# Kernel optimization log

Measured on AMD Instinct MI355X. Metric: run time of the kernel, lower is better.

Reference implementation:

```python
import jax, jax.numpy as jnp
import numpy as np

B, S, D, G, N_ORIG = 4, 4096, 512, 64, 4096
EPS_NORM = 1e-12   # F.normalize eps
EPS_MERGE = 1e-8   # merge-weight eps


def setup_inputs() -> dict:
    key = jax.random.key(0)
    k1, k2, k3 = jax.random.split(key, 3)
    x = jax.random.normal(k1, (B, S, D), dtype=jnp.float32)
    source = jax.random.uniform(k2, (B, S, N_ORIG), dtype=jnp.float32)
    position_ids = jnp.arange(B * S, dtype=jnp.int64).reshape(B, S)
    W = jax.random.normal(k3, (D, G), dtype=jnp.float32) * 0.05  # group_proj weight (no bias)
    return {"x": x, "source": source, "position_ids": position_ids,
            "r": 1024, "window_size": 16, "W": W}


def _token_merge(x, source, position_ids, r, window_size, W):
    Bb, Ss, Dd = x.shape
    r = min(r, Ss // 2)
    idx = jnp.arange(Ss, dtype=jnp.int32)
    # local candidate pairs: |i-j| = d for d in 1..window_size-1
    pi = jnp.concatenate([idx[:Ss - d] for d in range(1, min(window_size, Ss))])
    pj = jnp.concatenate([idx[d:] for d in range(1, min(window_size, Ss))])

    g = x @ W                                   # (B,S,G)
    norms = jnp.linalg.norm(g, axis=-1)         # (B,S)
    gn = g / jnp.maximum(norms, EPS_NORM)[..., None]
    sim = jnp.einsum('bpg,bpg->bp', gn[:, pi], gn[:, pj])  # (B,P)

    def greedy(sim_b):
        # deterministic order: score DESC, i ASC, j ASC
        order = jnp.lexsort((pj, pi, -sim_b))
        oi, oj = pi[order], pj[order]

        def step(carry, ij):
            used, partner, cnt = carry
            i, j = ij
            take = (cnt < r) & (~used[i]) & (~used[j])
            used = used.at[i].set(used[i] | take).at[j].set(used[j] | take)
            partner = partner.at[i].set(jnp.where(take, j, partner[i]))
            cnt = cnt + take.astype(jnp.int32)
            return (used, partner, cnt), None

        init = (jnp.zeros(Ss, bool), jnp.full(Ss, -1, jnp.int32), jnp.int32(0))
        (used, partner, cnt), _ = jax.lax.scan(step, init, (oi, oj))
        return partner  # partner[i] = j if pair (i,j) selected, else -1

    partner = jax.vmap(greedy)(sim)  # (B,S)

    def merge(xb, sb, pb, partner_b, norms_b):
        sel = partner_b >= 0
        pj_safe = jnp.where(sel, partner_b, idx)
        wi = norms_b
        wj = jnp.where(sel, norms_b[pj_safe], 0.0)
        merged = (wi[:, None] * xb + wj[:, None] * xb[pj_safe]) / (wi + wj + EPS_MERGE)[:, None]
        x_m = jnp.where(sel[:, None], merged, xb)
        s_m = sb + jnp.where(sel, 1.0, 0.0)[:, None] * sb[pj_safe]
        # drop the second token of each merged pair, preserving order
        skip_idx = jnp.where(sel, partner_b, Ss)
        skip = jnp.zeros(Ss, bool).at[skip_idx].set(True, mode='drop')
        keep = jnp.argsort(skip.astype(jnp.int8), stable=True)[: Ss - r]
        return x_m[keep], s_m[keep], pb[keep]

    return jax.vmap(merge)(x, source, position_ids, partner, norms)


def reference(x, source, position_ids, r, window_size, W):
    return _token_merge(x, source, position_ids, r, window_size, W)
```

## Files before the change

### kernel.cpp

```cpp
#include <hip/hip_runtime.h>

#define BATCH 4
#define SLEN 4096
#define DDIM 512
#define GDIM 64
#define NORIG 4096
#define WMAX 15
#define RSEL 1024
#define KEEP (SLEN - RSEL)
#define NTOK (BATCH * SLEN)
#define PEEL_ROUNDS 256
#define LDSL 16

typedef float __attribute__((ext_vector_type(4))) f32x4;

#define OFF_LISTS ((size_t)0)
#define OFF_GN    ((size_t)0)
#define OFF_SIMST ((size_t)8388608)
#define OFF_NORMS ((size_t)10485760)
#define OFF_KT    ((size_t)10584064)
#define OFF_PJR   ((size_t)10633216)
#define OFF_WIR   ((size_t)10682368)
#define OFF_WJR   ((size_t)10731520)
#define WS_NEEDED ((size_t)10780672)

#define OUTX_OFF 0
#define OUTS_OFF 6291456
#define OUTP_OFF 56623104

__global__ __launch_bounds__(256) void k_proj(const float* __restrict__ x,
                                              const float* __restrict__ Wm,
                                              double* __restrict__ gn,
                                              float* __restrict__ norms) {
  __shared__ float xs[16 * DDIM];
  int base = blockIdx.x * 16;
  const float4* src = (const float4*)(x + (size_t)base * DDIM);
  float4* dstv = (float4*)xs;
  for (int idx = threadIdx.x; idx < 16 * DDIM / 4; idx += 256) dstv[idx] = src[idx];
  __syncthreads();
  int lane = threadIdx.x & 63;
  int wv = threadIdx.x >> 6;
  double acc0 = 0, acc1 = 0, acc2 = 0, acc3 = 0;
  const float* xw = xs + wv * 4 * DDIM;
  for (int d = 0; d < DDIM; ++d) {
    double wval = (double)Wm[d * GDIM + lane];
    acc0 += (double)xw[d] * wval;
    acc1 += (double)xw[DDIM + d] * wval;
    acc2 += (double)xw[2 * DDIM + d] * wval;
    acc3 += (double)xw[3 * DDIM + d] * wval;
  }
  double accs[4] = {acc0, acc1, acc2, acc3};
  for (int k = 0; k < 4; ++k) {
    double a = accs[k];
    double ss = a * a;
    for (int o = 32; o >= 1; o >>= 1) ss += __shfl_xor(ss, o, 64);
    double nrm = sqrt(ss);
    int tok = base + wv * 4 + k;
    if (lane == 0) norms[tok] = (float)nrm;
    double denom = nrm > 1e-12 ? nrm : 1e-12;
    gn[(size_t)tok * GDIM + lane] = a / denom;
  }
}

__global__ __launch_bounds__(256) void k_sims(const double* __restrict__ gn,
                                              double* __restrict__ simsT) {
  int blk = blockIdx.x;
  int b = blk >> 6;
  int t0 = (blk & 63) * 64;
  int nrows = min(64 + WMAX, SLEN - t0);
  __shared__ double gs[(64 + WMAX) * GDIM];
  const double* src = gn + ((size_t)b * SLEN + t0) * GDIM;
  for (int idx = threadIdx.x; idx < nrows * GDIM; idx += 256) gs[idx] = src[idx];
  __syncthreads();
  int lane = threadIdx.x & 63, wv = threadIdx.x >> 6;
  for (int s = wv; s < 64 * WMAX; s += 4) {
    int il = s & 63, d = (s >> 6) + 1;
    int i = t0 + il;
    if (i + d < SLEN) {
      double p = gs[il * GDIM + lane] * gs[(il + d) * GDIM + lane];
      for (int o = 32; o >= 1; o >>= 1) p += __shfl_xor(p, o, 64);
      if (lane == 0) simsT[((size_t)(b * SLEN + i)) * 16 + d] = p;
    }
  }
}

__global__ __launch_bounds__(256) void k_lists(const double* __restrict__ simsT,
                                               signed char* __restrict__ lists8) {
  __shared__ signed char stage[4][32];
  int wave = threadIdx.x >> 6, lane = threadIdx.x & 63;
  int t = blockIdx.x * 4 + wave;
  int b = t >> 12, tt = t & (SLEN - 1);
  const double* sb = simsT + (size_t)b * SLEN * 16;
  int d = (lane >> 1) + 1;
  int side = lane & 1;
  bool valid = (lane < 30) && (side == 0 ? (tt + d < SLEN) : (tt - d >= 0));
  unsigned long long key = 0ULL;
  unsigned int code = 0xFFFFu;
  signed char delta = 0;
  if (valid) {
    int i = (side == 0) ? tt : (tt - d);
    double s = sb[(size_t)i * 16 + d];
    unsigned long long bits = (unsigned long long)__double_as_longlong(s);
    key = (bits & 0x8000000000000000ULL) ? ~bits : (bits | 0x8000000000000000ULL);
    code = (unsigned int)((i << 4) | d);
    delta = (side == 0) ? (signed char)d : (signed char)(-d);
  }
  int rank = 0;
#pragma clang loop unroll(disable)
  for (int q = 0; q < 30; ++q) {
    unsigned long long kq = __shfl(key, q, 64);
    unsigned int cq = __shfl(code, q, 64);
    if (kq != 0ULL && (kq > key || (kq == key && cq < code))) rank++;
  }
  if (lane < 32) stage[wave][lane] = 0;
  if (valid) stage[wave][rank] = delta;
  if (lane < 32) lists8[(size_t)t * 32 + lane] = stage[wave][lane];
}

__global__ __launch_bounds__(1024) void k_match(const signed char* __restrict__ lists8,
                                                const double* __restrict__ simsT_all,
                                                const float* __restrict__ norms,
                                                int* __restrict__ kt, int* __restrict__ pjr,
                                                float* __restrict__ wir, float* __restrict__ wjr,
                                                float* __restrict__ out_pos) {
  int b = blockIdx.x;
  const signed char* lb = lists8 + (size_t)b * SLEN * 32;
  const double* simsT = simsT_all + (size_t)b * SLEN * 16;
  __shared__ __align__(16) unsigned char big[65536];
  __shared__ signed char bp[SLEN];
  __shared__ unsigned char used[SLEN];
  __shared__ unsigned char cur[SLEN];
  __shared__ unsigned short takenCode[2048];
  __shared__ unsigned char meta[SLEN];
  __shared__ int takenCnt, baseCnt;
  __shared__ int sharedB, sharedNeed, sdone, allAccept, smallStraddle;
  __shared__ int memberCnt;
  __shared__ int wTot[16], wOff[16];
  signed char* l8 = (signed char*)big;
  int tid = threadIdx.x;

#pragma clang loop unroll(disable)
  for (int t = tid; t < SLEN; t += 1024) {
    const unsigned long long* lp = (const unsigned long long*)(lb + (size_t)t * 32);
    unsigned long long v0 = lp[0], v1 = lp[1];
    unsigned long long* dp = (unsigned long long*)(l8 + t * LDSL);
    dp[0] = v0; dp[1] = v1;
    bp[t] = (signed char)(v0 & 0xFF);
    used[t] = 0; cur[t] = 0; meta[t] = 0;
  }
  if (tid == 0) takenCnt = 0;
  __syncthreads();

#pragma clang loop unroll(disable)
  for (int round = 0; round < PEEL_ROUNDS; ++round) {
    if (tid == 0) baseCnt = takenCnt;
    __syncthreads();
#pragma clang loop unroll(disable)
    for (int t = tid; t < SLEN; t += 1024) {
      int dlt = bp[t];
      if (dlt > 0 && !used[t]) {
        int j = t + dlt;
        if (!used[j] && bp[j] == (signed char)(-dlt)) {
          int idx = atomicAdd(&takenCnt, 1);
          if (idx < 2048) takenCode[idx] = (unsigned short)((t << 4) | dlt);
          used[t] = 1; used[j] = 1;
        }
      }
    }
    __syncthreads();
    int newCnt = takenCnt;
    if (newCnt == baseCnt) break;
#pragma clang loop unroll(disable)
    for (int t = tid; t < SLEN; t += 1024) {
      if (used[t]) { bp[t] = 0; continue; }
      int dlt = bp[t];
      if (dlt == 0) continue;
      int p = t + dlt;
      int cc = cur[t];
#pragma clang loop unroll(disable)
      while (dlt != 0 && used[p]) {
        ++cc;
        dlt = (cc < LDSL) ? l8[t * LDSL + cc]
            : ((cc < 32) ? lb[(size_t)t * 32 + cc] : (signed char)0);
        p = t + dlt;
      }
      cur[t] = (unsigned char)cc;
      bp[t] = (signed char)dlt;
    }
    __syncthreads();
  }

  unsigned long long* key = (unsigned long long*)big;
  unsigned short* codeA = (unsigned short*)(big + 16384);
  unsigned char* state = (unsigned char*)(big + 20480);
  unsigned int* hist = (unsigned int*)(big + 22528);
  unsigned int* bcum = (unsigned int*)(big + 23552);
  unsigned int* wsum = (unsigned int*)(big + 24576);
  unsigned short* memberIdx = (unsigned short*)(big + 24704);
  int m = min(takenCnt, 2048);
  __syncthreads();
#pragma clang loop unroll(disable)
  for (int k = tid; k < m; k += 1024) {
    unsigned short c = takenCode[k];
    codeA[k] = c;
    state[k] = 0;
    double s = simsT[(size_t)(c >> 4) * 16 + (c & 15)];
    unsigned long long bits = (unsigned long long)__double_as_longlong(s);
    key[k] = (bits & 0x8000000000000000ULL) ? ~bits : (bits | 0x8000000000000000ULL);
  }
  if (tid == 0) { sharedNeed = RSEL; sdone = 0; allAccept = (m <= RSEL); smallStraddle = 0; memberCnt = 0; }
  __syncthreads();

  if (!allAccept) {
#pragma clang loop unroll(disable)
    for (int pass = 0; pass < 8; ++pass) {
      if (tid < 256) hist[tid] = 0;
      __syncthreads();
      int sh = 56 - 8 * pass;
#pragma clang loop unroll(disable)
      for (int k = tid; k < m; k += 1024)
        if (!state[k]) atomicAdd(&hist[(unsigned int)(key[k] >> sh) & 0xFFu], 1u);
      __syncthreads();
      unsigned int v = 0, inc = 0;
      int lane = tid & 63, w = tid >> 6;
      if (tid < 256) {
        v = hist[255 - tid];
        inc = v;
        for (int o = 1; o < 64; o <<= 1) { unsigned int n = __shfl_up(inc, o, 64); if (lane >= o) inc += n; }
        if (lane == 63) wsum[w] = inc;
      }
      __syncthreads();
      if (tid < 256) {
        unsigned int off = 0;
        for (int ww = 0; ww < w; ++ww) off += wsum[ww];
        unsigned int incl = inc + off;
        bcum[255 - tid] = incl - v;
      }
      __syncthreads();
      if (tid < 256) {
        int bkt = 255 - tid;
        unsigned int ag = bcum[bkt];
        unsigned int need = (unsigned int)sharedNeed;
        if (ag < need && ag + hist[bkt] >= need) sharedB = bkt;
      }
      __syncthreads();
      int B = sharedB;
      unsigned int needInB = (unsigned int)sharedNeed - bcum[B];
#pragma clang loop unroll(disable)
      for (int k = tid; k < m; k += 1024) {
        if (!state[k]) {
          unsigned int bv = (unsigned int)(key[k] >> sh) & 0xFFu;
          if ((int)bv > B) state[k] = 1;
          else if ((int)bv < B) state[k] = 2;
        }
      }
      __syncthreads();
      if (tid == 0) {
        sharedNeed = (int)needInB;
        if (hist[B] == needInB) sdone = 1;
        else if (hist[B] <= 128) smallStraddle = 1;
      }
      __syncthreads();
      if (sdone || smallStraddle) break;
    }
  }
  __syncthreads();

  if (allAccept || sdone) {
#pragma clang loop unroll(disable)
    for (int k = tid; k < m; k += 1024) if (!state[k]) state[k] = 1;
  } else {
#pragma clang loop unroll(disable)
    for (int k = tid; k < m; k += 1024)
      if (!state[k]) { int idx = atomicAdd(&memberCnt, 1); memberIdx[idx] = (unsigned short)k; }
    __syncthreads();
    int mc = memberCnt;
    unsigned int need = (unsigned int)sharedNeed;
#pragma clang loop unroll(disable)
    for (int z = tid; z < mc; z += 1024) {
      int k = memberIdx[z];
      unsigned long long kk = key[k];
      unsigned short ck = codeA[k];
      unsigned int wr = 0;
#pragma clang loop unroll(disable)
      for (int q2 = 0; q2 < mc; ++q2) {
        int q = memberIdx[q2];
        unsigned long long kq = key[q];
        if (kq > kk || (kq == kk && codeA[q] < ck)) wr++;
      }
      if (wr < need) state[k] = 1;
    }
  }
  __syncthreads();
#pragma clang loop unroll(disable)
  for (int k = tid; k < m; k += 1024) {
    if (state[k] == 1) {
      unsigned short ck = codeA[k];
      int i = ck >> 4, d = ck & 15;
      meta[i] = (unsigned char)d;
      meta[i + d] = 0x80;
    }
  }
  __syncthreads();
  int cnt = 0; unsigned char kf[4];
  int tbase = tid * 4;
  for (int u = 0; u < 4; ++u) { kf[u] = (meta[tbase + u] & 0x80) ? 0 : 1; cnt += kf[u]; }
  int lane = tid & 63, wv = tid >> 6;
  int incl = cnt;
  for (int o = 1; o < 64; o <<= 1) { int n = __shfl_up(incl, o, 64); if (lane >= o) incl += n; }
  if (lane == 63) wTot[wv] = incl;
  __syncthreads();
  if (tid < 16) {
    int v2 = wTot[tid];
    for (int o = 1; o < 16; o <<= 1) { int n = __shfl_up(v2, o, 64); if (lane >= o) v2 += n; }
    wOff[tid] = v2 - wTot[tid];
  }
  __syncthreads();
  int pos = wOff[wv] + (incl - cnt);
  for (int u = 0; u < 4; ++u) {
    int t = tbase + u;
    if (kf[u]) {
      if (pos < KEEP) {
        int orow = b * KEEP + pos;
        kt[orow] = t;
        int d = meta[t] & 15;
        pjr[orow] = d ? (t + d) : -1;
        wir[orow] = norms[b * SLEN + t];
        wjr[orow] = d ? norms[b * SLEN + t + d] : 0.0f;
        out_pos[orow] = (float)(b * SLEN + t);
      }
      pos++;
    }
  }
}

__global__ __launch_bounds__(256) void k_gather(const float* __restrict__ x,
                                                const float* __restrict__ src,
                                                const int* __restrict__ kt, const int* __restrict__ pjr,
                                                const float* __restrict__ wir, const float* __restrict__ wjr,
                                                float* __restrict__ outx, float* __restrict__ outs) {
  int orow = blockIdx.x;
  int b = orow / KEEP;
  int t = kt[orow], pj = pjr[orow];
  int gi = min(max(b * SLEN + t, 0), NTOK - 1);
  int gj = min(b * SLEN + min(max(pj, 0), SLEN - 1), NTOK - 1);
  int c = threadIdx.x;
  if (c < 128) {
    const f32x4* xi = (const f32x4*)(x + (size_t)gi * DDIM);
    f32x4 v = __builtin_nontemporal_load(&xi[c]);
    if (pj >= 0) {
      const f32x4* xj = (const f32x4*)(x + (size_t)gj * DDIM);
      f32x4 u = __builtin_nontemporal_load(&xj[c]);
      float wi = wir[orow], wj = wjr[orow];
      float inv = 1.0f / (wi + wj + 1e-8f);
      v = (v * wi + u * wj) * inv;
    }
    __builtin_nontemporal_store(v, (f32x4*)(outx + (size_t)orow * DDIM) + c);
  }
  const f32x4* si = (const f32x4*)(src + (size_t)gi * NORIG);
  f32x4* o = (f32x4*)(outs + (size_t)orow * NORIG);
  if (pj >= 0) {
    const f32x4* sj = (const f32x4*)(src + (size_t)gj * NORIG);
    for (int u = 0; u < 4; ++u) {
      int c2 = c + u * 256;
      f32x4 a = __builtin_nontemporal_load(&si[c2]);
      f32x4 bb = __builtin_nontemporal_load(&sj[c2]);
      __builtin_nontemporal_store(a + bb, &o[c2]);
    }
  } else {
    for (int u = 0; u < 4; ++u) {
      int c2 = c + u * 256;
      f32x4 a = __builtin_nontemporal_load(&si[c2]);
      __builtin_nontemporal_store(a, &o[c2]);
    }
  }
}

extern "C" void kernel_launch(void* const* d_in, const int* in_sizes, int n_in,
                              void* d_out, int out_size, void* d_ws, size_t ws_size,
                              hipStream_t stream) {
  if (ws_size < WS_NEEDED) return;

  const float* x = (const float*)d_in[0];
  const float* source = (const float*)d_in[1];
  const float* Wm = (const float*)d_in[5];

  char* ws = (char*)d_ws;
  double* gn = (double*)(ws + OFF_GN);
  double* simsT = (double*)(ws + OFF_SIMST);
  float* norms = (float*)(ws + OFF_NORMS);
  signed char* lists8 = (signed char*)(ws + OFF_LISTS);
  int* kt = (int*)(ws + OFF_KT);
  int* pjr = (int*)(ws + OFF_PJR);
  float* wir = (float*)(ws + OFF_WIR);
  float* wjr = (float*)(ws + OFF_WJR);

  float* out = (float*)d_out;
  float* outx = out + OUTX_OFF;
  float* outs = out + OUTS_OFF;
  float* outp = out + OUTP_OFF;

  k_proj<<<(BATCH * SLEN) / 16, 256, 0, stream>>>(x, Wm, gn, norms);
  k_sims<<<BATCH * (SLEN / 64), 256, 0, stream>>>(gn, simsT);
  k_lists<<<NTOK / 4, 256, 0, stream>>>(simsT, lists8);
  k_match<<<BATCH, 1024, 0, stream>>>(lists8, simsT, norms, kt, pjr, wir, wjr, outp);
  k_gather<<<BATCH * KEEP, 256, 0, stream>>>(x, source, kt, pjr, wir, wjr, outx, outs);
}
```

Measured before the change: 346.9 us.

## Split matching into single-wave peel kernel and separate ranking kernel

Result: slower. 889.7 us (+156.4%).

```diff
diff --git a/kernel.cpp b/kernel.cpp
--- a/kernel.cpp
+++ b/kernel.cpp
@@ -14,7 +14,9 @@
 
 typedef float __attribute__((ext_vector_type(4))) f32x4;
 
-#define OFF_LISTS ((size_t)0)
+#define OFF_TCODE ((size_t)0)
+#define OFF_TCNT  ((size_t)16384)
+#define OFF_LISTS ((size_t)32768)
 #define OFF_GN    ((size_t)0)
 #define OFF_SIMST ((size_t)8388608)
 #define OFF_NORMS ((size_t)10485760)
@@ -117,53 +119,50 @@
   if (lane < 32) lists8[(size_t)t * 32 + lane] = stage[wave][lane];
 }
 
-__global__ __launch_bounds__(1024) void k_match(const signed char* __restrict__ lists8,
-                                                const double* __restrict__ simsT_all,
-                                                const float* __restrict__ norms,
-                                                int* __restrict__ kt, int* __restrict__ pjr,
-                                                float* __restrict__ wir, float* __restrict__ wjr,
-                                                float* __restrict__ out_pos) {
+__global__ __launch_bounds__(64) void k_peel(const signed char* __restrict__ lists8,
+                                             unsigned short* __restrict__ tcodeG,
+                                             int* __restrict__ tcntG) {
   int b = blockIdx.x;
   const signed char* lb = lists8 + (size_t)b * SLEN * 32;
-  const double* simsT = simsT_all + (size_t)b * SLEN * 16;
-  __shared__ __align__(16) unsigned char big[65536];
+  __shared__ signed char l8[SLEN * LDSL];
   __shared__ signed char bp[SLEN];
-  __shared__ unsigned char used[SLEN];
+  __shared__ unsigned char usedA[SLEN];
   __shared__ unsigned char cur[SLEN];
   __shared__ unsigned short takenCode[2048];
-  __shared__ unsigned char meta[SLEN];
   __shared__ int takenCnt, baseCnt;
-  __shared__ int sharedB, sharedNeed, sdone, allAccept, smallStraddle;
-  __shared__ int memberCnt;
-  __shared__ int wTot[16], wOff[16];
-  signed char* l8 = (signed char*)big;
-  int tid = threadIdx.x;
-
-#pragma clang loop unroll(disable)
-  for (int t = tid; t < SLEN; t += 1024) {
+  int lane = threadIdx.x;
+#pragma clang loop unroll(disable)
+  for (int t = lane; t < SLEN; t += 64) {
     const unsigned long long* lp = (const unsigned long long*)(lb + (size_t)t * 32);
     unsigned long long v0 = lp[0], v1 = lp[1];
     unsigned long long* dp = (unsigned long long*)(l8 + t * LDSL);
     dp[0] = v0; dp[1] = v1;
     bp[t] = (signed char)(v0 & 0xFF);
-    used[t] = 0; cur[t] = 0; meta[t] = 0;
-  }
-  if (tid == 0) takenCnt = 0;
-  __syncthreads();
-
+    usedA[t] = 0; cur[t] = 0;
+  }
+  if (lane == 0) takenCnt = 0;
+  __syncthreads();
+
+  int tb = lane * 64;
 #pragma clang loop unroll(disable)
   for (int round = 0; round < PEEL_ROUNDS; ++round) {
-    if (tid == 0) baseCnt = takenCnt;
+    if (lane == 0) baseCnt = takenCnt;
     __syncthreads();
 #pragma clang loop unroll(disable)
-    for (int t = tid; t < SLEN; t += 1024) {
-      int dlt = bp[t];
-      if (dlt > 0 && !used[t]) {
-        int j = t + dlt;
-        if (!used[j] && bp[j] == (signed char)(-dlt)) {
-          int idx = atomicAdd(&takenCnt, 1);
-          if (idx < 2048) takenCode[idx] = (unsigned short)((t << 4) | dlt);
-          used[t] = 1; used[j] = 1;
+    for (int c8 = 0; c8 < 8; ++c8) {
+      unsigned long long w8 = *(const unsigned long long*)(bp + tb + c8 * 8);
+      if (w8 == 0ULL) continue;
+#pragma clang loop unroll(disable)
+      for (int u = 0; u < 8; ++u) {
+        signed char dlt = (signed char)(w8 >> (8 * u));
+        if (dlt > 0) {
+          int t = tb + c8 * 8 + u;
+          int j = t + dlt;
+          if (bp[j] == (signed char)(-dlt)) {
+            int idx = atomicAdd(&takenCnt, 1);
+            if (idx < 2048) takenCode[idx] = (unsigned short)((t << 4) | dlt);
+            usedA[t] = 1; usedA[j] = 1;
+          }
         }
       }
     }
@@ -171,37 +170,64 @@
     int newCnt = takenCnt;
     if (newCnt == baseCnt) break;
 #pragma clang loop unroll(disable)
-    for (int t = tid; t < SLEN; t += 1024) {
-      if (used[t]) { bp[t] = 0; continue; }
-      int dlt = bp[t];
-      if (dlt == 0) continue;
-      int p = t + dlt;
-      int cc = cur[t];
-#pragma clang loop unroll(disable)
-      while (dlt != 0 && used[p]) {
-        ++cc;
-        dlt = (cc < LDSL) ? l8[t * LDSL + cc]
-            : ((cc < 32) ? lb[(size_t)t * 32 + cc] : (signed char)0);
-        p = t + dlt;
-      }
-      cur[t] = (unsigned char)cc;
-      bp[t] = (signed char)dlt;
+    for (int c8 = 0; c8 < 8; ++c8) {
+      unsigned long long w8 = *(const unsigned long long*)(bp + tb + c8 * 8);
+      if (w8 == 0ULL) continue;
+#pragma clang loop unroll(disable)
+      for (int u = 0; u < 8; ++u) {
+        signed char dlt = (signed char)(w8 >> (8 * u));
+        if (dlt == 0) continue;
+        int t = tb + c8 * 8 + u;
+        if (usedA[t]) { bp[t] = 0; continue; }
+        int p = t + dlt;
+        int cc = cur[t];
+        bool adv = false;
+#pragma clang loop unroll(disable)
+        while (dlt != 0 && usedA[p]) {
+          ++cc; adv = true;
+          dlt = (cc < LDSL) ? l8[t * LDSL + cc]
+              : ((cc < 32) ? lb[(size_t)t * 32 + cc] : (signed char)0);
+          p = t + dlt;
+        }
+        if (adv) { cur[t] = (unsigned char)cc; bp[t] = dlt; }
+      }
     }
     __syncthreads();
   }
 
-  unsigned long long* key = (unsigned long long*)big;
-  unsigned short* codeA = (unsigned short*)(big + 16384);
-  unsigned char* state = (unsigned char*)(big + 20480);
-  unsigned int* hist = (unsigned int*)(big + 22528);
-  unsigned int* bcum = (unsigned int*)(big + 23552);
-  unsigned int* wsum = (unsigned int*)(big + 24576);
-  unsigned short* memberIdx = (unsigned short*)(big + 24704);
   int m = min(takenCnt, 2048);
-  __syncthreads();
+#pragma clang loop unroll(disable)
+  for (int k = lane; k < m; k += 64) tcodeG[b * 2048 + k] = takenCode[k];
+  if (lane == 0) tcntG[b] = m;
+}
+
+__global__ __launch_bounds__(1024) void k_rank(const double* __restrict__ simsT_all,
+                                               const unsigned short* __restrict__ tcodeG,
+                                               const int* __restrict__ tcntG,
+                                               const float* __restrict__ norms,
+                                               int* __restrict__ kt, int* __restrict__ pjr,
+                                               float* __restrict__ wir, float* __restrict__ wjr,
+                                               float* __restrict__ out_pos) {
+  int b = blockIdx.x;
+  const double* simsT = simsT_all + (size_t)b * SLEN * 16;
+  __shared__ unsigned long long key[2048];
+  __shared__ unsigned short codeA[2048];
+  __shared__ unsigned char state[2048];
+  __shared__ unsigned int hist[256];
+  __shared__ unsigned int bcum[256];
+  __shared__ unsigned int wsum[4];
+  __shared__ int sharedB, sharedNeed, sdone, allAccept, smallStraddle;
+  __shared__ unsigned short memberIdx[2048];
+  __shared__ int memberCnt;
+  __shared__ unsigned char meta[SLEN];
+  __shared__ int wTot[16], wOff[16];
+  int tid = threadIdx.x;
+  int m = min(tcntG[b], 2048);
+#pragma clang loop unroll(disable)
+  for (int t = tid; t < SLEN; t += 1024) meta[t] = 0;
 #pragma clang loop unroll(disable)
   for (int k = tid; k < m; k += 1024) {
-    unsigned short c = takenCode[k];
+    unsigned short c = tcodeG[b * 2048 + k];
     codeA[k] = c;
     state[k] = 0;
     double s = simsT[(size_t)(c >> 4) * 16 + (c & 15)];
@@ -389,6 +415,8 @@
   double* gn = (double*)(ws + OFF_GN);
   double* simsT = (double*)(ws + OFF_SIMST);
   float* norms = (float*)(ws + OFF_NORMS);
+  unsigned short* tcode = (unsigned short*)(ws + OFF_TCODE);
+  int* tcnt = (int*)(ws + OFF_TCNT);
   signed char* lists8 = (signed char*)(ws + OFF_LISTS);
   int* kt = (int*)(ws + OFF_KT);
   int* pjr = (int*)(ws + OFF_PJR);
@@ -403,6 +431,7 @@
   k_proj<<<(BATCH * SLEN) / 16, 256, 0, stream>>>(x, Wm, gn, norms);
   k_sims<<<BATCH * (SLEN / 64), 256, 0, stream>>>(gn, simsT);
   k_lists<<<NTOK / 4, 256, 0, stream>>>(simsT, lists8);
-  k_match<<<BATCH, 1024, 0, stream>>>(lists8, simsT, norms, kt, pjr, wir, wjr, outp);
+  k_peel<<<BATCH, 64, 0, stream>>>(lists8, tcode, tcnt);
+  k_rank<<<BATCH, 1024, 0, stream>>>(simsT, tcode, tcnt, norms, kt, pjr, wir, wjr, outp);
   k_gather<<<BATCH * KEEP, 256, 0, stream>>>(x, source, kt, pjr, wir, wjr, outx, outs);
 }
```

## Cache full 32-entry candidate lists in LDS and pack peel loop by four tokens

Applied to the files above, without the earlier changes.

After: 331.5 us (median of 2 runs). 4.5% less time.

```diff
diff --git a/kernel.cpp b/kernel.cpp
--- a/kernel.cpp
+++ b/kernel.cpp
@@ -10,7 +10,7 @@
 #define KEEP (SLEN - RSEL)
 #define NTOK (BATCH * SLEN)
 #define PEEL_ROUNDS 256
-#define LDSL 16
+#define LDSL 32
 
 typedef float __attribute__((ext_vector_type(4))) f32x4;
 
@@ -126,9 +126,9 @@
   int b = blockIdx.x;
   const signed char* lb = lists8 + (size_t)b * SLEN * 32;
   const double* simsT = simsT_all + (size_t)b * SLEN * 16;
-  __shared__ __align__(16) unsigned char big[65536];
-  __shared__ signed char bp[SLEN];
-  __shared__ unsigned char used[SLEN];
+  __shared__ __align__(16) unsigned char big[SLEN * LDSL];
+  __shared__ __align__(8) signed char bp[SLEN];
+  __shared__ unsigned char usedA[SLEN];
   __shared__ unsigned char cur[SLEN];
   __shared__ unsigned short takenCode[2048];
   __shared__ unsigned char meta[SLEN];
@@ -142,50 +142,62 @@
 #pragma clang loop unroll(disable)
   for (int t = tid; t < SLEN; t += 1024) {
     const unsigned long long* lp = (const unsigned long long*)(lb + (size_t)t * 32);
-    unsigned long long v0 = lp[0], v1 = lp[1];
+    unsigned long long v0 = lp[0], v1 = lp[1], v2 = lp[2], v3 = lp[3];
     unsigned long long* dp = (unsigned long long*)(l8 + t * LDSL);
-    dp[0] = v0; dp[1] = v1;
+    dp[0] = v0; dp[1] = v1; dp[2] = v2; dp[3] = v3;
     bp[t] = (signed char)(v0 & 0xFF);
-    used[t] = 0; cur[t] = 0; meta[t] = 0;
+    usedA[t] = 0; cur[t] = 0; meta[t] = 0;
   }
   if (tid == 0) takenCnt = 0;
   __syncthreads();
 
+  int tb4 = tid * 4;
 #pragma clang loop unroll(disable)
   for (int round = 0; round < PEEL_ROUNDS; ++round) {
     if (tid == 0) baseCnt = takenCnt;
     __syncthreads();
-#pragma clang loop unroll(disable)
-    for (int t = tid; t < SLEN; t += 1024) {
-      int dlt = bp[t];
-      if (dlt > 0 && !used[t]) {
-        int j = t + dlt;
-        if (!used[j] && bp[j] == (signed char)(-dlt)) {
-          int idx = atomicAdd(&takenCnt, 1);
-          if (idx < 2048) takenCode[idx] = (unsigned short)((t << 4) | dlt);
-          used[t] = 1; used[j] = 1;
+    {
+      unsigned int w4 = *(const unsigned int*)(bp + tb4);
+      if (w4 != 0u) {
+#pragma clang loop unroll(disable)
+        for (int u = 0; u < 4; ++u) {
+          signed char dlt = (signed char)(w4 >> (8 * u));
+          if (dlt > 0) {
+            int t = tb4 + u;
+            int j = t + dlt;
+            if (bp[j] == (signed char)(-dlt)) {
+              int idx = atomicAdd(&takenCnt, 1);
+              if (idx < 2048) takenCode[idx] = (unsigned short)((t << 4) | dlt);
+              usedA[t] = 1; usedA[j] = 1;
+            }
+          }
         }
       }
     }
     __syncthreads();
     int newCnt = takenCnt;
     if (newCnt == baseCnt) break;
-#pragma clang loop unroll(disable)
-    for (int t = tid; t < SLEN; t += 1024) {
-      if (used[t]) { bp[t] = 0; continue; }
-      int dlt = bp[t];
-      if (dlt == 0) continue;
-      int p = t + dlt;
-      int cc = cur[t];
-#pragma clang loop unroll(disable)
-      while (dlt != 0 && used[p]) {
-        ++cc;
-        dlt = (cc < LDSL) ? l8[t * LDSL + cc]
-            : ((cc < 32) ? lb[(size_t)t * 32 + cc] : (signed char)0);
-        p = t + dlt;
-      }
-      cur[t] = (unsigned char)cc;
-      bp[t] = (signed char)dlt;
+    {
+      unsigned int w4 = *(const unsigned int*)(bp + tb4);
+      if (w4 != 0u) {
+#pragma clang loop unroll(disable)
+        for (int u = 0; u < 4; ++u) {
+          signed char dlt = (signed char)(w4 >> (8 * u));
+          if (dlt == 0) continue;
+          int t = tb4 + u;
+          if (usedA[t]) { bp[t] = 0; continue; }
+          int p = t + dlt;
+          int cc = cur[t];
+          bool adv = false;
+#pragma clang loop unroll(disable)
+          while (dlt != 0 && usedA[p]) {
+            ++cc; adv = true;
+            dlt = (cc < LDSL) ? l8[t * LDSL + cc] : (signed char)0;
+            p = t + dlt;
+          }
+          if (adv) { cur[t] = (unsigned char)cc; bp[t] = dlt; }
+        }
+      }
     }
     __syncthreads();
   }
```
